# Performance work log

Hardware: AMD Instinct MI355X
Metric: run time of the kernel (lower is better)

Reference implementation:

```python
import jax, jax.numpy as jnp
import numpy as np

B, IN, OUT, H = 32768, 512, 512, 8
DH = OUT // H
SCALE = float(np.sqrt(DH))


def setup_inputs() -> dict:
    key = jax.random.key(0)
    ks = jax.random.split(key, 10)
    inp = {
        "protein_features": jax.random.normal(ks[0], (B, IN), jnp.float32),
        "ligand_features": jax.random.normal(ks[1], (B, IN), jnp.float32),
    }
    names = ["q1", "k1", "v1", "q2", "k2", "v2", "o1", "o2"]
    for i, n in enumerate(names):
        fan_in = IN if n[0] in "qkv" else OUT
        kw, kb = jax.random.split(ks[2 + i])
        inp[f"W{n}"] = jax.random.normal(kw, (OUT, fan_in), jnp.float32) * 0.02
        inp[f"b{n}"] = jax.random.normal(kb, (OUT,), jnp.float32) * 0.02
    return inp


def _attend(q, k, v):
    # q,k,v: [B, 1, H, DH]. Original code does matmul(q, k.transpose(-2,-1))
    # WITHOUT moving heads to a batch axis, so attention mixes the H heads
    # of each sample: scores [B, 1, H, H], softmax over last axis.
    scores = jnp.einsum('bshd,bsed->bshe', q, k) / SCALE
    attn = jax.nn.softmax(scores, axis=-1)
    return jnp.einsum('bshe,bsed->bshd', attn, v)  # [B,1,H,DH]


def reference(protein_features, ligand_features,
              Wq1, bq1, Wk1, bk1, Wv1, bv1,
              Wq2, bq2, Wk2, bk2, Wv2, bv2,
              Wo1, bo1, Wo2, bo2):
    Bn = protein_features.shape[0]

    def proj(x, W, b):  # torch Linear: x @ W^T + b, then view(B, -1, H, DH)
        return (x @ W.T + b).reshape(Bn, -1, H, DH)

    q1 = proj(protein_features, Wq1, bq1)
    k1 = proj(ligand_features, Wk1, bk1)
    v1 = proj(ligand_features, Wv1, bv1)
    q2 = proj(ligand_features, Wq2, bq2)
    k2 = proj(protein_features, Wk2, bk2)
    v2 = proj(protein_features, Wv2, bv2)

    out1 = _attend(q1, k1, v1).reshape(Bn, -1)  # [B, OUT]
    out2 = _attend(q2, k2, v2).reshape(Bn, -1)  # [B, OUT]
    protein_output = out1 @ Wo1.T + bo1
    ligand_output = out2 @ Wo2.T + bo2
    return (protein_output, ligand_output)
```

## Files before the change

kernel.cpp:

```cpp
#include <hip/hip_runtime.h>
#include <hip/hip_bf16.h>

#define B_ROWS 32768
#define K_DIM  512
#define NP     1536

typedef __attribute__((ext_vector_type(8))) short          bf16x8;
typedef __attribute__((ext_vector_type(8))) unsigned short u16x8;
typedef __attribute__((ext_vector_type(4))) unsigned short u16x4;
typedef __attribute__((ext_vector_type(4))) float          f32x4;

static __device__ __forceinline__ unsigned short f2bf(float f) {
  __hip_bfloat16 h = __float2bfloat16(f);
  unsigned short u; __builtin_memcpy(&u, &h, 2); return u;
}
static __device__ __forceinline__ float bf2f(unsigned short u) {
  unsigned int x = ((unsigned int)u) << 16; float f; __builtin_memcpy(&f, &x, 4); return f;
}

static __device__ __forceinline__ void gload_lds16(const void* g, void* l) {
  __builtin_amdgcn_global_load_lds(
      (const __attribute__((address_space(1))) void*)g,
      (__attribute__((address_space(3))) void*)l, 16, 0, 0);
}

__global__ __launch_bounds__(256) void pack_kernel(
    const float* __restrict__ Wq1, const float* __restrict__ Wk1,
    const float* __restrict__ Wv1, const float* __restrict__ Wq2,
    const float* __restrict__ Wk2, const float* __restrict__ Wv2,
    const float* __restrict__ Wo1, const float* __restrict__ Wo2,
    const float* __restrict__ bq1, const float* __restrict__ bk1,
    const float* __restrict__ bv1, const float* __restrict__ bq2,
    const float* __restrict__ bk2, const float* __restrict__ bv2,
    unsigned short* __restrict__ Wp, unsigned short* __restrict__ Wl,
    unsigned short* __restrict__ Wo1b, unsigned short* __restrict__ Wo2b,
    float* __restrict__ bp, float* __restrict__ bl)
{
  const int gid = blockIdx.x * 256 + threadIdx.x;
  const int idx = gid * 4;
  const float* src; unsigned short* dst;
  if (idx < 786432) {
    int n = idx >> 9, k = idx & 511;
    const float* W = (n < 512) ? (Wq1 + (size_t)n * 512)
                   : (n < 1024) ? (Wk2 + (size_t)(n - 512) * 512)
                                : (Wv2 + (size_t)(n - 1024) * 512);
    src = W + k; dst = Wp + idx;
  } else if (idx < 1572864) {
    int r = idx - 786432; int n = r >> 9, k = r & 511;
    const float* W = (n < 512) ? (Wk1 + (size_t)n * 512)
                   : (n < 1024) ? (Wv1 + (size_t)(n - 512) * 512)
                                : (Wq2 + (size_t)(n - 1024) * 512);
    src = W + k; dst = Wl + r;
  } else if (idx < 1835008) {
    int r = idx - 1572864; src = Wo1 + r; dst = Wo1b + r;
  } else {
    int r = idx - 1835008; src = Wo2 + r; dst = Wo2b + r;
  }
  float4 v = *reinterpret_cast<const float4*>(src);
  u16x4 o; o[0] = f2bf(v.x); o[1] = f2bf(v.y); o[2] = f2bf(v.z); o[3] = f2bf(v.w);
  *reinterpret_cast<u16x4*>(dst) = o;

  if (gid < 1536) {
    int n = gid;
    bp[n] = (n < 512) ? bq1[n] : (n < 1024) ? bk2[n - 512] : bv2[n - 1024];
  } else if (gid < 3072) {
    int n = gid - 1536;
    bl[n] = (n < 512) ? bk1[n] : (n < 1024) ? bv1[n - 512] : bq2[n - 1024];
  }
}

__global__ __launch_bounds__(256) void cvt_kernel(
    const float* __restrict__ xp, const float* __restrict__ xl,
    unsigned short* __restrict__ xpb, unsigned short* __restrict__ xlb)
{
  const size_t gid = (size_t)blockIdx.x * 256 + threadIdx.x;
  size_t i = gid * 8;
  const float* src; unsigned short* dst;
  if (i < 16777216) { src = xp + i; dst = xpb + i; }
  else              { src = xl + (i - 16777216); dst = xlb + (i - 16777216); }
  float4 a = ((const float4*)src)[0];
  float4 b = ((const float4*)src)[1];
  u16x8 o;
  o[0] = f2bf(a.x); o[1] = f2bf(a.y); o[2] = f2bf(a.z); o[3] = f2bf(a.w);
  o[4] = f2bf(b.x); o[5] = f2bf(b.y); o[6] = f2bf(b.z); o[7] = f2bf(b.w);
  *(u16x8*)dst = o;
}

template<bool OUT_F32>
__global__ __launch_bounds__(256, 2)
void gemm_kernel(const unsigned short* __restrict__ Aptr, int lda,
                 const unsigned short* __restrict__ Wb,
                 const float* __restrict__ bias,
                 void* __restrict__ Cptr, int ldc,
                 int ntiles)
{
  __shared__ __align__(16) unsigned short As[128 * 32];
  __shared__ __align__(16) unsigned short Bs[128 * 32];

  const int nwg = gridDim.x;
  const int cpx = nwg >> 3;
  const int b0  = blockIdx.x;
  const int wk  = (b0 & 7) * cpx + (b0 >> 3);
  const int mt  = wk / ntiles, nt = wk - mt * ntiles;
  const int m0  = mt << 7, n0 = nt << 7;

  const int tid = threadIdx.x;
  const int lane = tid & 63, w = tid >> 6;
  const int wm = w >> 1, wn = w & 1;
  const int fr = lane & 15, fk = lane >> 4;

  f32x4 acc[4][4] = {};

  for (int kk = 0; kk < 512; kk += 32) {
#pragma unroll
    for (int r = 0; r < 2; ++r) {
      const int t = r * 256 + tid;
      gload_lds16(Wb + (size_t)(n0 + (t >> 2)) * 512 + kk + (t & 3) * 8,
                  &Bs[r * 2048 + w * 512]);
    }
#pragma unroll
    for (int r = 0; r < 2; ++r) {
      const int t = r * 256 + tid;
      gload_lds16(Aptr + (size_t)(m0 + (t >> 2)) * lda + kk + (t & 3) * 8,
                  &As[r * 2048 + w * 512]);
    }
    __syncthreads();

    bf16x8 af[4], bfr[4];
#pragma unroll
    for (int i = 0; i < 4; ++i) {
      af[i]  = *(const bf16x8*)&As[(wm * 64 + i * 16 + fr) * 32 + fk * 8];
      bfr[i] = *(const bf16x8*)&Bs[(wn * 64 + i * 16 + fr) * 32 + fk * 8];
    }
#pragma unroll
    for (int mi = 0; mi < 4; ++mi)
#pragma unroll
      for (int ni = 0; ni < 4; ++ni)
        acc[mi][ni] = __builtin_amdgcn_mfma_f32_16x16x32_bf16(af[mi], bfr[ni], acc[mi][ni], 0, 0, 0);
    __syncthreads();
  }

#pragma unroll
  for (int ni = 0; ni < 4; ++ni) {
    const int col = n0 + wn * 64 + ni * 16 + fr;
    const float bv = bias[col];
#pragma unroll
    for (int mi = 0; mi < 4; ++mi) {
      const int rbase = m0 + wm * 64 + mi * 16 + fk * 4;
#pragma unroll
      for (int j = 0; j < 4; ++j) {
        const float v = acc[mi][ni][j] + bv;
        if (OUT_F32)
          ((float*)Cptr)[(size_t)(rbase + j) * ldc + col] = v;
        else
          ((unsigned short*)Cptr)[(size_t)(rbase + j) * ldc + col] = f2bf(v);
      }
    }
  }
}

__global__ __launch_bounds__(256, 4)
void attn_kernel(unsigned short* __restrict__ qkvp, unsigned short* __restrict__ qkvl)
{
  __shared__ float lds[4][1696];
  const int w = threadIdx.x >> 6, lane = threadIdx.x & 63;
  const size_t r = (size_t)blockIdx.x * 4 + w;
  unsigned short* rp = qkvp + r * NP;
  unsigned short* rl = qkvl + r * NP;
  const int l8 = lane * 8;

  u16x8 q1 = *(const u16x8*)(rp + l8);
  u16x8 k2 = *(const u16x8*)(rp + 512 + l8);
  u16x8 v2 = *(const u16x8*)(rp + 1024 + l8);
  u16x8 k1 = *(const u16x8*)(rl + l8);
  u16x8 v1 = *(const u16x8*)(rl + 512 + l8);
  u16x8 q2 = *(const u16x8*)(rl + 1024 + l8);

  float* Q   = &lds[w][0];
  float* Kk  = Q + 544;
  float* V   = Kk + 544;
  float* ATT = V + 544;
  const int h = lane >> 3, e = lane & 7;
  const int sb = h * 68 + (lane & 7) * 8;

  auto stage = [&](u16x8 qv, u16x8 kv, u16x8 vv) {
#pragma unroll
    for (int j = 0; j < 8; ++j) {
      Q [sb + j] = bf2f((unsigned short)qv[j]);
      Kk[sb + j] = bf2f((unsigned short)kv[j]);
      V [sb + j] = bf2f((unsigned short)vv[j]);
    }
  };
  auto attend = [&](unsigned short* outp) {
    float s = 0.f;
#pragma unroll
    for (int d = 0; d < 64; ++d) s += Q[h * 68 + d] * Kk[e * 68 + d];
    s *= 0.125f;
    float m = fmaxf(s, __shfl_xor(s, 1, 8));
    m = fmaxf(m, __shfl_xor(m, 2, 8));
    m = fmaxf(m, __shfl_xor(m, 4, 8));
    const float p = __expf(s - m);
    float su = p;
    su += __shfl_xor(su, 1, 8); su += __shfl_xor(su, 2, 8); su += __shfl_xor(su, 4, 8);
    ATT[lane] = p / su;
    float o[8];
    const int d0 = (lane & 7) * 8;
#pragma unroll
    for (int j = 0; j < 8; ++j) {
      float a = 0.f;
#pragma unroll
      for (int e2 = 0; e2 < 8; ++e2) a += ATT[h * 8 + e2] * V[e2 * 68 + d0 + j];
      o[j] = a;
    }
    u16x8 ob;
#pragma unroll
    for (int j = 0; j < 8; ++j) ob[j] = f2bf(o[j]);
    *(u16x8*)(outp + l8) = ob;
  };

  stage(q1, k1, v1);
  attend(rp);
  stage(q2, k2, v2);
  attend(rl);
}

extern "C" void kernel_launch(void* const* d_in, const int* in_sizes, int n_in,
                              void* d_out, int out_size, void* d_ws, size_t ws_size,
                              hipStream_t stream)
{
  const float* xp  = (const float*)d_in[0];
  const float* xl  = (const float*)d_in[1];
  const float* Wq1 = (const float*)d_in[2];   const float* bq1 = (const float*)d_in[3];
  const float* Wk1 = (const float*)d_in[4];   const float* bk1 = (const float*)d_in[5];
  const float* Wv1 = (const float*)d_in[6];   const float* bv1 = (const float*)d_in[7];
  const float* Wq2 = (const float*)d_in[8];   const float* bq2 = (const float*)d_in[9];
  const float* Wk2 = (const float*)d_in[10];  const float* bk2 = (const float*)d_in[11];
  const float* Wv2 = (const float*)d_in[12];  const float* bv2 = (const float*)d_in[13];
  const float* Wo1 = (const float*)d_in[14];  const float* bo1 = (const float*)d_in[15];
  const float* Wo2 = (const float*)d_in[16];  const float* bo2 = (const float*)d_in[17];

  char* p = (char*)d_ws;
  unsigned short* Wp   = (unsigned short*)p; p += (size_t)786432 * 2;
  unsigned short* Wl   = (unsigned short*)p; p += (size_t)786432 * 2;
  unsigned short* Wo1b = (unsigned short*)p; p += (size_t)262144 * 2;
  unsigned short* Wo2b = (unsigned short*)p; p += (size_t)262144 * 2;
  float*          bp   = (float*)p;          p += (size_t)1536 * 4;
  float*          bl   = (float*)p;          p += (size_t)1536 * 4;
  unsigned short* qkvp = (unsigned short*)p; p += (size_t)B_ROWS * NP * 2;
  unsigned short* qkvl = (unsigned short*)p; p += (size_t)B_ROWS * NP * 2;
  (void)ws_size; (void)in_sizes; (void)n_in; (void)out_size;

  unsigned short* xpb = (unsigned short*)d_out;
  unsigned short* xlb = xpb + (size_t)B_ROWS * 512;

  pack_kernel<<<2048, 256, 0, stream>>>(Wq1, Wk1, Wv1, Wq2, Wk2, Wv2, Wo1, Wo2,
                                        bq1, bk1, bv1, bq2, bk2, bv2,
                                        Wp, Wl, Wo1b, Wo2b, bp, bl);
  cvt_kernel<<<16384, 256, 0, stream>>>(xp, xl, xpb, xlb);

  gemm_kernel<false><<<3072, 256, 0, stream>>>(xpb, 512, Wp, bp, qkvp, NP, 12);
  gemm_kernel<false><<<3072, 256, 0, stream>>>(xlb, 512, Wl, bl, qkvl, NP, 12);

  attn_kernel<<<8192, 256, 0, stream>>>(qkvp, qkvl);

  float* out_p = (float*)d_out;
  float* out_l = out_p + (size_t)B_ROWS * 512;
  gemm_kernel<true><<<1024, 256, 0, stream>>>(qkvp, NP, Wo1b, bo1, out_p, 512, 4);
  gemm_kernel<true><<<1024, 256, 0, stream>>>(qkvl, NP, Wo2b, bo2, out_l, 512, 4);
}
```

Measured before the change: 502.2 us.

## Replace GEMM with 8-wave 256x128 tile, triple-buffered LDS pipeline and swizzle

Rewrites the projection GEMM kernel to use 512-thread blocks computing 256x128 tiles with BK=64, a three-stage LDS ring buffer fed by async global-to-LDS loads, and an XOR-swizzled LDS layout. The MFMA work is split into two half-tiles with barriers, priority boosts and partial waitcnts so loads of future stages overlap compute. It targets memory latency stalls and LDS bank conflicts in the old single-buffered kernel. In exchange it uses about 144 KB of dynamic LDS, which limits residency to one block per CU.

```diff
diff --git a/kernel.cpp b/kernel.cpp
--- a/kernel.cpp
+++ b/kernel.cpp
@@ -87,58 +87,114 @@
 }
 
 template<bool OUT_F32>
-__global__ __launch_bounds__(256, 2)
-void gemm_kernel(const unsigned short* __restrict__ Aptr, int lda,
-                 const unsigned short* __restrict__ Wb,
-                 const float* __restrict__ bias,
-                 void* __restrict__ Cptr, int ldc,
-                 int ntiles)
-{
-  __shared__ __align__(16) unsigned short As[128 * 32];
-  __shared__ __align__(16) unsigned short Bs[128 * 32];
-
-  const int nwg = gridDim.x;
-  const int cpx = nwg >> 3;
-  const int b0  = blockIdx.x;
-  const int wk  = (b0 & 7) * cpx + (b0 >> 3);
-  const int mt  = wk / ntiles, nt = wk - mt * ntiles;
-  const int m0  = mt << 7, n0 = nt << 7;
+__global__ __launch_bounds__(512, 2)
+void gemm8p(const unsigned short* __restrict__ Aptr, int lda,
+            const unsigned short* __restrict__ Wb,
+            const float* __restrict__ bias,
+            void* __restrict__ Cptr, int ldc, int ntiles)
+{
+  extern __shared__ __align__(16) unsigned short lds[];
+  const int SLOT = 24576, BOFF = 16384;
+
+  const int nwg = gridDim.x, cpx = nwg >> 3, b0 = blockIdx.x;
+  const int wk = (b0 & 7) * cpx + (b0 >> 3);
+  const int mt = wk / ntiles, nt = wk - mt * ntiles;
+  const int m0 = mt << 8, n0 = nt << 7;
 
   const int tid = threadIdx.x;
   const int lane = tid & 63, w = tid >> 6;
   const int wm = w >> 1, wn = w & 1;
-  const int fr = lane & 15, fk = lane >> 4;
+  const int fr = lane & 15, fk = lane >> 4, frx = fr & 7;
+
+  const int r8 = tid >> 3;
+  const int k8 = (tid & 7) ^ (r8 & 7);
+  const unsigned short* Ab = Aptr + (size_t)(m0 + r8) * lda + k8 * 8;
+  const unsigned short* Bb = Wb  + (size_t)(n0 + r8) * 512 + k8 * 8;
+  const int ldsW = w * 512;
+
+  const int koff0 = ((0 + fk) ^ frx) * 8;
+  const int koff1 = ((4 + fk) ^ frx) * 8;
 
   f32x4 acc[4][4] = {};
 
-  for (int kk = 0; kk < 512; kk += 32) {
-#pragma unroll
-    for (int r = 0; r < 2; ++r) {
-      const int t = r * 256 + tid;
-      gload_lds16(Wb + (size_t)(n0 + (t >> 2)) * 512 + kk + (t & 3) * 8,
-                  &Bs[r * 2048 + w * 512]);
-    }
-#pragma unroll
-    for (int r = 0; r < 2; ++r) {
-      const int t = r * 256 + tid;
-      gload_lds16(Aptr + (size_t)(m0 + (t >> 2)) * lda + kk + (t & 3) * 8,
-                  &As[r * 2048 + w * 512]);
-    }
-    __syncthreads();
-
-    bf16x8 af[4], bfr[4];
-#pragma unroll
-    for (int i = 0; i < 4; ++i) {
-      af[i]  = *(const bf16x8*)&As[(wm * 64 + i * 16 + fr) * 32 + fk * 8];
-      bfr[i] = *(const bf16x8*)&Bs[(wn * 64 + i * 16 + fr) * 32 + fk * 8];
-    }
-#pragma unroll
-    for (int mi = 0; mi < 4; ++mi)
+#define STAGE_A(kt, s, j) \
+  gload_lds16(Ab + (size_t)(kt) * 64 + (size_t)(j) * 64 * lda, \
+              &lds[(s) * SLOT + (j) * 4096 + ldsW])
+#define STAGE_B(kt, s, j) \
+  gload_lds16(Bb + (size_t)(kt) * 64 + (size_t)(j) * 64 * 512, \
+              &lds[(s) * SLOT + BOFF + (j) * 4096 + ldsW])
+
+  STAGE_A(0, 0, 0); STAGE_A(0, 0, 1); STAGE_A(0, 0, 2); STAGE_A(0, 0, 3);
+  STAGE_B(0, 0, 0); STAGE_B(0, 0, 1);
+  STAGE_A(1, 1, 0); STAGE_A(1, 1, 1); STAGE_A(1, 1, 2); STAGE_A(1, 1, 3);
+  STAGE_B(1, 1, 0); STAGE_B(1, 1, 1);
+  asm volatile("s_waitcnt vmcnt(6)" ::: "memory");
+  __builtin_amdgcn_s_barrier();
+
+  int rd = 0;
+  for (int t = 0; t < 8; ++t) {
+    const int As_ = rd * SLOT, Bs_ = rd * SLOT + BOFF;
+    const int st  = rd ? rd - 1 : 2;
+    const bool pre = (t < 6);
+
+    bf16x8 bfr[4][2], afq[2][2];
+#pragma unroll
+    for (int ni = 0; ni < 4; ++ni) {
+      const int rb = Bs_ + (wn * 64 + ni * 16 + fr) * 64;
+      bfr[ni][0] = *(const bf16x8*)&lds[rb + koff0];
+      bfr[ni][1] = *(const bf16x8*)&lds[rb + koff1];
+    }
+#pragma unroll
+    for (int m2 = 0; m2 < 2; ++m2) {
+      const int ra = As_ + (wm * 64 + m2 * 16 + fr) * 64;
+      afq[m2][0] = *(const bf16x8*)&lds[ra + koff0];
+      afq[m2][1] = *(const bf16x8*)&lds[ra + koff1];
+    }
+    if (pre) { STAGE_A(t + 2, st, 0); STAGE_A(t + 2, st, 1); STAGE_A(t + 2, st, 2); }
+    asm volatile("s_waitcnt lgkmcnt(8)" ::: "memory");
+    __builtin_amdgcn_s_barrier();
+    asm volatile("s_waitcnt lgkmcnt(0)" ::: "memory");
+    __builtin_amdgcn_sched_barrier(0);
+    __builtin_amdgcn_s_setprio(1);
+#pragma unroll
+    for (int m2 = 0; m2 < 2; ++m2)
 #pragma unroll
       for (int ni = 0; ni < 4; ++ni)
-        acc[mi][ni] = __builtin_amdgcn_mfma_f32_16x16x32_bf16(af[mi], bfr[ni], acc[mi][ni], 0, 0, 0);
-    __syncthreads();
+#pragma unroll
+        for (int kc = 0; kc < 2; ++kc)
+          acc[m2][ni] = __builtin_amdgcn_mfma_f32_16x16x32_bf16(
+              afq[m2][kc], bfr[ni][kc], acc[m2][ni], 0, 0, 0);
+    __builtin_amdgcn_s_setprio(0);
+    __builtin_amdgcn_s_barrier();
+
+#pragma unroll
+    for (int m2 = 0; m2 < 2; ++m2) {
+      const int ra = As_ + (wm * 64 + 32 + m2 * 16 + fr) * 64;
+      afq[m2][0] = *(const bf16x8*)&lds[ra + koff0];
+      afq[m2][1] = *(const bf16x8*)&lds[ra + koff1];
+    }
+    if (pre) { STAGE_A(t + 2, st, 3); STAGE_B(t + 2, st, 0); STAGE_B(t + 2, st, 1); }
+    if (pre)            asm volatile("s_waitcnt vmcnt(6)" ::: "memory");
+    else if (t == 6)    asm volatile("s_waitcnt vmcnt(0)" ::: "memory");
+    __builtin_amdgcn_s_barrier();
+    asm volatile("s_waitcnt lgkmcnt(0)" ::: "memory");
+    __builtin_amdgcn_sched_barrier(0);
+    __builtin_amdgcn_s_setprio(1);
+#pragma unroll
+    for (int m2 = 0; m2 < 2; ++m2)
+#pragma unroll
+      for (int ni = 0; ni < 4; ++ni)
+#pragma unroll
+        for (int kc = 0; kc < 2; ++kc)
+          acc[2 + m2][ni] = __builtin_amdgcn_mfma_f32_16x16x32_bf16(
+              afq[m2][kc], bfr[ni][kc], acc[2 + m2][ni], 0, 0, 0);
+    __builtin_amdgcn_s_setprio(0);
+    __builtin_amdgcn_s_barrier();
+
+    rd = (rd + 1 == 3) ? 0 : rd + 1;
   }
+#undef STAGE_A
+#undef STAGE_B
 
 #pragma unroll
   for (int ni = 0; ni < 4; ++ni) {
@@ -253,18 +309,24 @@
   unsigned short* xpb = (unsigned short*)d_out;
   unsigned short* xlb = xpb + (size_t)B_ROWS * 512;
 
+  const int LDSB = 147456;
+  hipFuncSetAttribute((const void*)gemm8p<false>,
+                      hipFuncAttributeMaxDynamicSharedMemorySize, LDSB);
+  hipFuncSetAttribute((const void*)gemm8p<true>,
+                      hipFuncAttributeMaxDynamicSharedMemorySize, LDSB);
+
   pack_kernel<<<2048, 256, 0, stream>>>(Wq1, Wk1, Wv1, Wq2, Wk2, Wv2, Wo1, Wo2,
                                         bq1, bk1, bv1, bq2, bk2, bv2,
                                         Wp, Wl, Wo1b, Wo2b, bp, bl);
   cvt_kernel<<<16384, 256, 0, stream>>>(xp, xl, xpb, xlb);
 
-  gemm_kernel<false><<<3072, 256, 0, stream>>>(xpb, 512, Wp, bp, qkvp, NP, 12);
-  gemm_kernel<false><<<3072, 256, 0, stream>>>(xlb, 512, Wl, bl, qkvl, NP, 12);
+  gemm8p<false><<<1536, 512, LDSB, stream>>>(xpb, 512, Wp, bp, qkvp, NP, 12);
+  gemm8p<false><<<1536, 512, LDSB, stream>>>(xlb, 512, Wl, bl, qkvl, NP, 12);
 
   attn_kernel<<<8192, 256, 0, stream>>>(qkvp, qkvl);
 
   float* out_p = (float*)d_out;
   float* out_l = out_p + (size_t)B_ROWS * 512;
-  gemm_kernel<true><<<1024, 256, 0, stream>>>(qkvp, NP, Wo1b, bo1, out_p, 512, 4);
-  gemm_kernel<true><<<1024, 256, 0, stream>>>(qkvl, NP, Wo2b, bo2, out_l, 512, 4);
-}
+  gemm8p<true><<<512, 512, LDSB, stream>>>(qkvp, NP, Wo1b, bo1, out_p, 512, 4);
+  gemm8p<true><<<512, 512, LDSB, stream>>>(qkvl, NP, Wo2b, bo2, out_l, 512, 4);
+}
```

Measured after the change: 502.5 us. Within noise of the previous version (+0.1%).
